# Optimization experiments

Hardware: AMD Instinct MI355X
Metric: run time of the kernel (lower is better)

The kernel has to match this reference:

```python
import jax, jax.numpy as jnp
import numpy as np

N_NODES = 50000


def _gcn_conv(x, src, dst, W, b, n_nodes):
    # x: [N, Fin] -> h: [N, Fout]; GCN: D^-1/2 (A+I) D^-1/2 (x W) + b
    h = x @ W
    deg = jax.ops.segment_sum(jnp.ones_like(dst, dtype=h.dtype), dst,
                              num_segments=n_nodes)
    dinv = jax.lax.rsqrt(jnp.maximum(deg, 1.0))
    norm = dinv[src] * dinv[dst]                      # [E]
    msg = h[src] * norm[:, None]                      # [E, Fout] gather
    agg = jax.ops.segment_sum(msg, dst, num_segments=n_nodes)  # scatter-add
    return agg + b


def setup_inputs() -> dict:
    key = jax.random.key(0)
    k0, k1, k2, k3 = jax.random.split(key, 4)
    N, E, F_IN, H, C = N_NODES, 800000, 128, 128, 16
    x = jax.random.normal(k0, (N, F_IN), dtype=jnp.float32)
    edge_index = jax.random.randint(k1, (2, E), 0, N, dtype=jnp.int64)
    W1 = jax.random.normal(k2, (F_IN, H), dtype=jnp.float32) / np.sqrt(F_IN)
    b1 = jnp.zeros((H,), dtype=jnp.float32)
    W2 = jax.random.normal(k3, (H, C), dtype=jnp.float32) / np.sqrt(H)
    b2 = jnp.zeros((C,), dtype=jnp.float32)
    return {"x": x, "edge_index": edge_index, "W1": W1, "b1": b1,
            "W2": W2, "b2": b2}


def reference(x, edge_index, W1, b1, W2, b2):
    n = x.shape[0]
    # add self-loops (shared by both conv layers)
    loops = jnp.arange(n, dtype=edge_index.dtype)
    src = jnp.concatenate([edge_index[0], loops])
    dst = jnp.concatenate([edge_index[1], loops])
    h = _gcn_conv(x, src, dst, W1, b1, n)
    h = jax.nn.relu(h)
    # dropout p=0.5 is identity in eval mode
    h = _gcn_conv(h, src, dst, W2, b2, n)
    return jax.nn.log_softmax(h, axis=1)
```

## Files before the change

### kernel.cpp

```cpp
#include <hip/hip_runtime.h>
#include <hip/hip_fp16.h>
#include <math.h>


#define NBUCKET_SHIFT 8
#define BIN_CHUNK 4096
#define PAD_SLOP (7 << NBUCKET_SHIFT)
#define CAP  5120
#define CCAP (CAP + PAD_SLOP)

typedef __bf16 bf16x8 __attribute__((ext_vector_type(8)));
typedef float  f32x4  __attribute__((ext_vector_type(4)));
typedef float  f32x2  __attribute__((ext_vector_type(2)));

__device__ __forceinline__ unsigned short pack_bf16(float f) {
    unsigned u = __float_as_uint(f);
    return (unsigned short)((u + 0x7fffu + ((u >> 16) & 1u)) >> 16);
}

__device__ __forceinline__ void acc_fp8x16_fma(f32x2* a, uint4 v, float w) {
    f32x2 ww; ww.x = w; ww.y = w;
    a[0] += __builtin_amdgcn_cvt_pk_f32_fp8(v.x, false) * ww;
    a[1] += __builtin_amdgcn_cvt_pk_f32_fp8(v.x, true)  * ww;
    a[2] += __builtin_amdgcn_cvt_pk_f32_fp8(v.y, false) * ww;
    a[3] += __builtin_amdgcn_cvt_pk_f32_fp8(v.y, true)  * ww;
    a[4] += __builtin_amdgcn_cvt_pk_f32_fp8(v.z, false) * ww;
    a[5] += __builtin_amdgcn_cvt_pk_f32_fp8(v.z, true)  * ww;
    a[6] += __builtin_amdgcn_cvt_pk_f32_fp8(v.w, false) * ww;
    a[7] += __builtin_amdgcn_cvt_pk_f32_fp8(v.w, true)  * ww;
}

__device__ __forceinline__ void acc_fp16x8(f32x2* a, uint4 v) {
    float2 f;
    f = __half22float2(*(const __half2*)&v.x); a[0] += *(f32x2*)&f;
    f = __half22float2(*(const __half2*)&v.y); a[1] += *(f32x2*)&f;
    f = __half22float2(*(const __half2*)&v.z); a[2] += *(f32x2*)&f;
    f = __half22float2(*(const __half2*)&v.w); a[3] += *(f32x2*)&f;
}

union K1Smem {
    struct { unsigned spair[BIN_CHUNK]; int lcnt[256]; int lbase[256]; } b;
    unsigned short wtp[16384];
    float outb[4][16 * 132];
};

__global__ __launch_bounds__(256)
void bin_gemm1_kernel(const int* __restrict__ src, const int* __restrict__ dst,
                      int* __restrict__ bcur, unsigned* __restrict__ pairs,
                      int E, int nbuckets, int nbins,
                      const float* __restrict__ x, const float* __restrict__ W1,
                      unsigned* __restrict__ h1b, int N) {
    __shared__ K1Smem sm;
    const int blk = blockIdx.x;
    const int tid = threadIdx.x;

    if (blk < nbins) {
        const int e0 = blk * BIN_CHUNK;
        const int cnt = min(BIN_CHUNK, E - e0);
        sm.b.lcnt[tid] = 0;
        __syncthreads();
        for (int i = tid; i < cnt; i += 256) {
            unsigned s = (unsigned)src[e0 + i], d = (unsigned)dst[e0 + i];
            sm.b.spair[i] = (d >> NBUCKET_SHIFT) << 24 | (d & 255u) << 16 | s;
            atomicAdd(&sm.b.lcnt[d >> NBUCKET_SHIFT], 1);
        }
        __syncthreads();
        if (tid < nbuckets) {
            int c = sm.b.lcnt[tid];
            sm.b.lbase[tid] = (c > 0) ? atomicAdd(&bcur[tid], c) : 0;
            sm.b.lcnt[tid] = 0;
        }
        __syncthreads();
        for (int i = tid; i < cnt; i += 256) {
            unsigned p = sm.b.spair[i];
            int b = (int)(p >> 24);
            int off = atomicAdd(&sm.b.lcnt[b], 1);
            pairs[b * CAP + sm.b.lbase[b] + off] = p;
        }
        return;
    }

    const int gblk = blk - nbins;
    const int wave = tid >> 6, lane = tid & 63;
    const int q = lane >> 4, m = lane & 15;
    const int row0 = gblk * 64 + wave * 16;
    const int row = row0 + m;
    const int rowc = (row < N) ? row : (N - 1);

    for (int it = tid; it < 16384; it += 256) {
        int k = it >> 7, n = it & 127;
        int t = n >> 4, mm = n & 15;
        int ks = k >> 5;
        int lane2 = (((k & 31) >> 3) << 4) | mm;
        int j = k & 7;
        sm.wtp[(t * 4 + ks) * 512 + lane2 * 8 + j] = pack_bf16(W1[it]);
    }
    __syncthreads();

    f32x4 acc[8];
#pragma unroll
    for (int t = 0; t < 8; t++) acc[t] = (f32x4)0.0f;

#pragma unroll
    for (int ks = 0; ks < 4; ks++) {
        const float4* xp = (const float4*)(x + (size_t)rowc * 128 + ks * 32 + q * 8);
        float4 f0 = xp[0], f1 = xp[1];
        float fv[8] = {f0.x, f0.y, f0.z, f0.w, f1.x, f1.y, f1.z, f1.w};
        bf16x8 ah;
#pragma unroll
        for (int j = 0; j < 8; j++) ah[j] = (__bf16)fv[j];
#pragma unroll
        for (int t = 0; t < 8; t++) {
            bf16x8 b = *(const bf16x8*)(sm.wtp + (size_t)(t * 4 + ks) * 512 + lane * 8);
            acc[t] = __builtin_amdgcn_mfma_f32_16x16x32_bf16(ah, b, acc[t], 0, 0, 0);
        }
    }
    __syncthreads();

#pragma unroll
    for (int t = 0; t < 8; t++)
#pragma unroll
        for (int r = 0; r < 4; r++)
            sm.outb[wave][(q * 4 + r) * 132 + t * 16 + m] = acc[t][r];
    __syncthreads();

    const int r2 = lane >> 2, j = lane & 3;
    const int orow = row0 + r2;
    if (orow < N) {
        const float* lrow = &sm.outb[wave][r2 * 132];
#pragma unroll
        for (int s = 0; s < 4; s++) {
            float4 a = *(const float4*)(lrow + s * 32 + j * 8);
            float4 b = *(const float4*)(lrow + s * 32 + j * 8 + 4);
            unsigned lo = __builtin_amdgcn_cvt_pk_fp8_f32(a.x, a.y, 0, false);
            lo = __builtin_amdgcn_cvt_pk_fp8_f32(a.z, a.w, lo, true);
            unsigned hi = __builtin_amdgcn_cvt_pk_fp8_f32(b.x, b.y, 0, false);
            hi = __builtin_amdgcn_cvt_pk_fp8_f32(b.z, b.w, hi, true);
            ((uint2*)h1b)[((size_t)(s >> 1) * (N + 1) + orow) * 8 + (s & 1) * 4 + j]
                = make_uint2(lo, hi);
        }
    }
}

__global__ __launch_bounds__(256)
void bucket_build_kernel(const int* __restrict__ bcur, const unsigned* __restrict__ pairs,
                         int* __restrict__ rowptr, int* __restrict__ rowcnt,
                         float* __restrict__ dinv, int* __restrict__ colsrc,
                         unsigned* __restrict__ h1b, int N, int nbuckets) {
    __shared__ int cnt[256];
    __shared__ int sm[256];
    const int tid = threadIdx.x;
    const int blk = blockIdx.x;
    const int nb0 = blk << NBUCKET_SHIFT;

    if (blk == 0) {
        if (tid < 16) h1b[((size_t)0 * (N + 1) + N) * 16 + tid] = 0u;
        else if (tid < 32) h1b[((size_t)1 * (N + 1) + N) * 16 + (tid - 16)] = 0u;
        else if (tid == 32) dinv[N] = 0.0f;
    }

    const int lo = blk * CAP;
    const int hi = lo + bcur[blk];
    cnt[tid] = 0;
    __syncthreads();

    for (int i = lo + tid; i < hi; i += 256)
        atomicAdd(&cnt[(int)(pairs[i] >> 16) & 255], 1);
    __syncthreads();

    int v = cnt[tid];
    int pdeg = (v + 7) & ~7;
    sm[tid] = pdeg;
    __syncthreads();
#pragma unroll
    for (int off = 1; off < 256; off <<= 1) {
        int u = (tid >= off) ? sm[tid - off] : 0;
        __syncthreads();
        sm[tid] += u;
        __syncthreads();
    }
    int pexcl = sm[tid] - pdeg;
    const int start = blk * CCAP + pexcl;
    int node = nb0 + tid;
    if (node < N) {
        rowptr[node] = start;
        rowcnt[node] = pdeg;
        dinv[node] = rsqrtf((float)v + 1.0f);
    }
    __syncthreads();
    cnt[tid] = start;
    __syncthreads();
    for (int i = lo + tid; i < hi; i += 256) {
        unsigned p = pairs[i];
        int pos = atomicAdd(&cnt[(int)(p >> 16) & 255], 1);
        colsrc[pos] = (int)(p & 0xffffu);
    }
    for (int p = start + v; p < start + pdeg; ++p)
        colsrc[p] = N;
}

__global__ __launch_bounds__(256)
void l1_fused_kernel(const int* __restrict__ rowptr, const int* __restrict__ rowcnt,
                     const int* __restrict__ colsrc,
                     const float* __restrict__ dinv, const unsigned* __restrict__ h1b,
                     const float* __restrict__ b1, const float* __restrict__ W2,
                     float* __restrict__ h2acc, int N) {
    __shared__ float rows[4][4][68];
    __shared__ float w2s[64 * 16];
    const int tid = threadIdx.x;
    const int wave = tid >> 6, lane = tid & 63;
    const int c = lane & 3;
    const int g = (lane >> 2) & 3;
    const int n = lane >> 4;
    const int p = blockIdx.x & 1;
    const int d = (blockIdx.x >> 1) * 16 + wave * 4 + n;

    for (int i = tid; i < 256; i += 256)
        ((float4*)w2s)[i] = ((const float4*)W2)[p * 256 + i];

    const uint4* hq = (const uint4*)h1b + (size_t)p * (N + 1) * 4;

    if (d < N) {
        const float dvd = dinv[d];
        f32x2 a[8];
#pragma unroll
        for (int j = 0; j < 8; j++) a[j] = (f32x2)0.0f;

        if (g == 0)
            acc_fp8x16_fma(a, hq[(size_t)d * 4 + c], dvd);

        int i = rowptr[d];
        const int end = i + rowcnt[d];
        int s0 = 0, s1 = 0, s2 = 0, s3 = 0;
        if (i + 16 <= end) {
            s0 = colsrc[i + g];      s1 = colsrc[i + g + 4];
            s2 = colsrc[i + g + 8];  s3 = colsrc[i + g + 12];
        }
        while (i + 16 <= end) {
            uint4 v0 = hq[(size_t)s0 * 4 + c];
            uint4 v1 = hq[(size_t)s1 * 4 + c];
            uint4 v2 = hq[(size_t)s2 * 4 + c];
            uint4 v3 = hq[(size_t)s3 * 4 + c];
            float w0 = dinv[s0], w1 = dinv[s1], w2 = dinv[s2], w3 = dinv[s3];
            i += 16;
            if (i + 16 <= end) {
                s0 = colsrc[i + g];      s1 = colsrc[i + g + 4];
                s2 = colsrc[i + g + 8];  s3 = colsrc[i + g + 12];
            }
            acc_fp8x16_fma(a, v0, w0); acc_fp8x16_fma(a, v1, w1);
            acc_fp8x16_fma(a, v2, w2); acc_fp8x16_fma(a, v3, w3);
        }
        for (; i + 4 <= end; i += 4) {
            int sx = colsrc[i + g];
            acc_fp8x16_fma(a, hq[(size_t)sx * 4 + c], dinv[sx]);
        }

#pragma unroll
        for (int j = 0; j < 8; j++) {
            a[j].x += __shfl_xor(a[j].x, 4, 64);
            a[j].y += __shfl_xor(a[j].y, 4, 64);
            a[j].x += __shfl_xor(a[j].x, 8, 64);
            a[j].y += __shfl_xor(a[j].y, 8, 64);
        }

        if (g == 0) {
            float* rbase = &rows[wave][n][c * 16];
#pragma unroll
            for (int t = 0; t < 4; t++) {
                float4 bb = ((const float4*)b1)[p * 16 + c * 4 + t];
                float4 o;
                o.x = fmaxf(a[2 * t].x * dvd + bb.x, 0.0f);
                o.y = fmaxf(a[2 * t].y * dvd + bb.y, 0.0f);
                o.z = fmaxf(a[2 * t + 1].x * dvd + bb.z, 0.0f);
                o.w = fmaxf(a[2 * t + 1].y * dvd + bb.w, 0.0f);
                *(float4*)(rbase + 4 * t) = o;
            }
        }
    }
    __syncthreads();

    const int n2 = lane >> 4, col = lane & 15;
    const int d2 = (blockIdx.x >> 1) * 16 + wave * 4 + n2;
    if (d2 < N) {
        const float* r = &rows[wave][n2][0];
        float p0 = 0.0f, p1 = 0.0f;
#pragma unroll
        for (int k = 0; k < 32; k++) {
            p0 = fmaf(r[k],      w2s[k * 16 + col],        p0);
            p1 = fmaf(r[k + 32], w2s[(k + 32) * 16 + col], p1);
        }
        atomicAdd(&h2acc[(size_t)d2 * 16 + col], p0 + p1);
    }
}

__global__ __launch_bounds__(256)
void h2cvt_kernel(const float* __restrict__ h2acc, const float* __restrict__ dinv,
                  unsigned* __restrict__ h2h, int N) {
    int idx = blockIdx.x * 256 + threadIdx.x;
    if (idx >= (N + 1) * 4) return;
    float dv = dinv[idx >> 2];
    float4 v = ((const float4*)h2acc)[idx];
    __half2 lo = __floats2half2_rn(v.x * dv, v.y * dv);
    __half2 hi = __floats2half2_rn(v.z * dv, v.w * dv);
    ((uint2*)h2h)[idx] = make_uint2(*(unsigned*)&lo, *(unsigned*)&hi);
}

__global__ __launch_bounds__(256)
void l2_kernel(const int* __restrict__ rowptr, const int* __restrict__ rowcnt,
               const int* __restrict__ colsrc,
               const float* __restrict__ dinv, const unsigned* __restrict__ h2s,
               const float* __restrict__ b2, float* __restrict__ out, int N) {
    const int tid = threadIdx.x;
    const int wave = tid >> 6, lane = tid & 63;
    const int n = lane >> 4;
    const int g = (lane >> 1) & 7;
    const int c = lane & 1;
    const int d = blockIdx.x * 16 + wave * 4 + n;
    if (d >= N) return;
    const uint4* h2q = (const uint4*)h2s;

    f32x2 a[4];
#pragma unroll
    for (int j = 0; j < 4; j++) a[j] = (f32x2)0.0f;

    if (g == 0)
        acc_fp16x8(a, h2q[(size_t)d * 2 + c]);

    int i = rowptr[d];
    const int end = i + rowcnt[d];
    uint4 v; int s2 = 0;
    if (i < end) {
        int s = colsrc[i + g];
        v = h2q[(size_t)s * 2 + c];
    }
    if (i + 8 < end) s2 = colsrc[i + 8 + g];
    while (i < end) {
        uint4 vc = v;
        if (i + 8 < end) v = h2q[(size_t)s2 * 2 + c];
        if (i + 16 < end) s2 = colsrc[i + 16 + g];
        i += 8;
        acc_fp16x8(a, vc);
    }

#pragma unroll
    for (int j = 0; j < 4; j++) {
#pragma unroll
        for (int off = 2; off <= 8; off <<= 1) {
            a[j].x += __shfl_xor(a[j].x, off, 64);
            a[j].y += __shfl_xor(a[j].y, off, 64);
        }
    }

    const float dv = dinv[d];
    const float* af = (const float*)a;
    float v8[8];
#pragma unroll
    for (int j = 0; j < 8; j++) v8[j] = af[j] * dv + b2[c * 8 + j];

    float m = v8[0];
#pragma unroll
    for (int j = 1; j < 8; j++) m = fmaxf(m, v8[j]);
    m = fmaxf(m, __shfl_xor(m, 1, 64));
    float e = 0.0f;
#pragma unroll
    for (int j = 0; j < 8; j++) e += expf(v8[j] - m);
    e += __shfl_xor(e, 1, 64);
    float lse = m + logf(e);

    if (g == 0) {
        float4 o0 = make_float4(v8[0] - lse, v8[1] - lse, v8[2] - lse, v8[3] - lse);
        float4 o1 = make_float4(v8[4] - lse, v8[5] - lse, v8[6] - lse, v8[7] - lse);
        float4* op = (float4*)(out + (size_t)d * 16 + c * 8);
        op[0] = o0; op[1] = o1;
    }
}

extern "C" void kernel_launch(void* const* d_in, const int* in_sizes, int n_in,
                              void* d_out, int out_size, void* d_ws, size_t ws_size,
                              hipStream_t stream) {
    const float* x  = (const float*)d_in[0];
    const int*  ei  = (const int*)d_in[1];
    const float* W1 = (const float*)d_in[2];
    const float* b1 = (const float*)d_in[3];
    const float* W2 = (const float*)d_in[4];
    const float* b2 = (const float*)d_in[5];
    float* out = (float*)d_out;

    const int N = in_sizes[0] / 128;
    const int E = in_sizes[1] / 2;
    const int* src = ei;
    const int* dst = ei + E;
    const int nbuckets = (N + 255) >> NBUCKET_SHIFT;
    const int nbins = (E + BIN_CHUNK - 1) / BIN_CHUNK;
    const int g1blocks = (N + 63) / 64;

    float*          wsf     = (float*)d_ws;
    float*          dinv    = wsf;
    int*            rowptr  = (int*)(wsf + N + 16);
    int*            rowcnt  = rowptr + N;
    int*            bcur    = rowcnt + N;
    float*          h2acc   = (float*)(bcur + 256);
    int*            colsrc  = (int*)(h2acc + (size_t)(N + 1) * 16);
    unsigned*       pairs   = (unsigned*)(colsrc + (size_t)nbuckets * CCAP);
    unsigned*       h1b     = pairs + (size_t)nbuckets * CAP;
    unsigned*       h2h     = pairs;

    hipMemsetAsync(bcur, 0, (256 + (size_t)(N + 1) * 16) * sizeof(int), stream);
    bin_gemm1_kernel<<<nbins + g1blocks, 256, 0, stream>>>(src, dst, bcur, pairs,
                                                           E, nbuckets, nbins,
                                                           x, W1, h1b, N);

    bucket_build_kernel<<<nbuckets, 256, 0, stream>>>(bcur, pairs, rowptr, rowcnt,
                                                      dinv, colsrc, h1b, N, nbuckets);

    l1_fused_kernel<<<((N + 15) / 16) * 2, 256, 0, stream>>>(rowptr, rowcnt, colsrc,
                                                             dinv, h1b, b1, W2,
                                                             h2acc, N);

    h2cvt_kernel<<<((N + 1) * 4 + 255) / 256, 256, 0, stream>>>(h2acc, dinv, h2h, N);

    l2_kernel<<<(N + 15) / 16, 256, 0, stream>>>(rowptr, rowcnt, colsrc, dinv, h2h,
                                                 b2, out, N);
}
```

Before: 158.4 us.

## Pack fp16 source norm weight into CSR column entries and precompute degrees

Degrees are now counted with global atomics during edge binning, so the bucket builder no longer makes its own counting pass over the pairs. Each CSR column entry now packs the 16-bit source index with an fp16 copy of that source's inverse-sqrt degree. The layer-1 gather then reads the weight from the column word instead of making a separate random dinv lookup. This trades 800K extra global atomics and an fp16 rounding of the edge weights for one fewer dependent gather per edge.

```diff
diff --git a/kernel.cpp b/kernel.cpp
--- a/kernel.cpp
+++ b/kernel.cpp
@@ -16,6 +16,10 @@
 __device__ __forceinline__ unsigned short pack_bf16(float f) {
     unsigned u = __float_as_uint(f);
     return (unsigned short)((u + 0x7fffu + ((u >> 16) & 1u)) >> 16);
+}
+
+__device__ __forceinline__ float unpack_w(unsigned u) {
+    return __half2float(__ushort_as_half((unsigned short)(u >> 16)));
 }
 
 __device__ __forceinline__ void acc_fp8x16_fma(f32x2* a, uint4 v, float w) {
@@ -47,7 +51,7 @@
 __global__ __launch_bounds__(256)
 void bin_gemm1_kernel(const int* __restrict__ src, const int* __restrict__ dst,
                       int* __restrict__ bcur, unsigned* __restrict__ pairs,
-                      int E, int nbuckets, int nbins,
+                      int* __restrict__ deg, int E, int nbuckets, int nbins,
                       const float* __restrict__ x, const float* __restrict__ W1,
                       unsigned* __restrict__ h1b, int N) {
     __shared__ K1Smem sm;
@@ -63,6 +67,7 @@
             unsigned s = (unsigned)src[e0 + i], d = (unsigned)dst[e0 + i];
             sm.b.spair[i] = (d >> NBUCKET_SHIFT) << 24 | (d & 255u) << 16 | s;
             atomicAdd(&sm.b.lcnt[d >> NBUCKET_SHIFT], 1);
+            atomicAdd(&deg[d], 1);
         }
         __syncthreads();
         if (tid < nbuckets) {
@@ -144,8 +149,9 @@
 
 __global__ __launch_bounds__(256)
 void bucket_build_kernel(const int* __restrict__ bcur, const unsigned* __restrict__ pairs,
+                         const int* __restrict__ deg,
                          int* __restrict__ rowptr, int* __restrict__ rowcnt,
-                         float* __restrict__ dinv, int* __restrict__ colsrc,
+                         float* __restrict__ dinv, unsigned* __restrict__ colsrc,
                          unsigned* __restrict__ h1b, int N, int nbuckets) {
     __shared__ int cnt[256];
     __shared__ int sm[256];
@@ -161,14 +167,9 @@
 
     const int lo = blk * CAP;
     const int hi = lo + bcur[blk];
-    cnt[tid] = 0;
-    __syncthreads();
-
-    for (int i = lo + tid; i < hi; i += 256)
-        atomicAdd(&cnt[(int)(pairs[i] >> 16) & 255], 1);
-    __syncthreads();
-
-    int v = cnt[tid];
+
+    int node = nb0 + tid;
+    int v = (node < N) ? deg[node] : 0;
     int pdeg = (v + 7) & ~7;
     sm[tid] = pdeg;
     __syncthreads();
@@ -181,7 +182,6 @@
     }
     int pexcl = sm[tid] - pdeg;
     const int start = blk * CCAP + pexcl;
-    int node = nb0 + tid;
     if (node < N) {
         rowptr[node] = start;
         rowcnt[node] = pdeg;
@@ -192,16 +192,19 @@
     __syncthreads();
     for (int i = lo + tid; i < hi; i += 256) {
         unsigned p = pairs[i];
+        unsigned s = p & 0xffffu;
         int pos = atomicAdd(&cnt[(int)(p >> 16) & 255], 1);
-        colsrc[pos] = (int)(p & 0xffffu);
+        float w = rsqrtf((float)deg[s] + 1.0f);
+        unsigned w16 = (unsigned)__half_as_ushort(__float2half_rn(w));
+        colsrc[pos] = s | (w16 << 16);
     }
     for (int p = start + v; p < start + pdeg; ++p)
-        colsrc[p] = N;
+        colsrc[p] = (unsigned)N;
 }
 
 __global__ __launch_bounds__(256)
 void l1_fused_kernel(const int* __restrict__ rowptr, const int* __restrict__ rowcnt,
-                     const int* __restrict__ colsrc,
+                     const unsigned* __restrict__ colsrc,
                      const float* __restrict__ dinv, const unsigned* __restrict__ h1b,
                      const float* __restrict__ b1, const float* __restrict__ W2,
                      float* __restrict__ h2acc, int N) {
@@ -231,28 +234,29 @@
 
         int i = rowptr[d];
         const int end = i + rowcnt[d];
-        int s0 = 0, s1 = 0, s2 = 0, s3 = 0;
+        unsigned u0 = 0, u1 = 0, u2 = 0, u3 = 0;
         if (i + 16 <= end) {
-            s0 = colsrc[i + g];      s1 = colsrc[i + g + 4];
-            s2 = colsrc[i + g + 8];  s3 = colsrc[i + g + 12];
+            u0 = colsrc[i + g];      u1 = colsrc[i + g + 4];
+            u2 = colsrc[i + g + 8];  u3 = colsrc[i + g + 12];
         }
         while (i + 16 <= end) {
-            uint4 v0 = hq[(size_t)s0 * 4 + c];
-            uint4 v1 = hq[(size_t)s1 * 4 + c];
-            uint4 v2 = hq[(size_t)s2 * 4 + c];
-            uint4 v3 = hq[(size_t)s3 * 4 + c];
-            float w0 = dinv[s0], w1 = dinv[s1], w2 = dinv[s2], w3 = dinv[s3];
+            uint4 v0 = hq[(size_t)(u0 & 0xffffu) * 4 + c];
+            uint4 v1 = hq[(size_t)(u1 & 0xffffu) * 4 + c];
+            uint4 v2 = hq[(size_t)(u2 & 0xffffu) * 4 + c];
+            uint4 v3 = hq[(size_t)(u3 & 0xffffu) * 4 + c];
+            float w0 = unpack_w(u0), w1 = unpack_w(u1);
+            float w2 = unpack_w(u2), w3 = unpack_w(u3);
             i += 16;
             if (i + 16 <= end) {
-                s0 = colsrc[i + g];      s1 = colsrc[i + g + 4];
-                s2 = colsrc[i + g + 8];  s3 = colsrc[i + g + 12];
+                u0 = colsrc[i + g];      u1 = colsrc[i + g + 4];
+                u2 = colsrc[i + g + 8];  u3 = colsrc[i + g + 12];
             }
             acc_fp8x16_fma(a, v0, w0); acc_fp8x16_fma(a, v1, w1);
             acc_fp8x16_fma(a, v2, w2); acc_fp8x16_fma(a, v3, w3);
         }
         for (; i + 4 <= end; i += 4) {
-            int sx = colsrc[i + g];
-            acc_fp8x16_fma(a, hq[(size_t)sx * 4 + c], dinv[sx]);
+            unsigned ux = colsrc[i + g];
+            acc_fp8x16_fma(a, hq[(size_t)(ux & 0xffffu) * 4 + c], unpack_w(ux));
         }
 
 #pragma unroll
@@ -307,7 +311,7 @@
 
 __global__ __launch_bounds__(256)
 void l2_kernel(const int* __restrict__ rowptr, const int* __restrict__ rowcnt,
-               const int* __restrict__ colsrc,
+               const unsigned* __restrict__ colsrc,
                const float* __restrict__ dinv, const unsigned* __restrict__ h2s,
                const float* __restrict__ b2, float* __restrict__ out, int N) {
     const int tid = threadIdx.x;
@@ -328,16 +332,16 @@
 
     int i = rowptr[d];
     const int end = i + rowcnt[d];
-    uint4 v; int s2 = 0;
+    uint4 v; unsigned u2 = 0;
     if (i < end) {
-        int s = colsrc[i + g];
-        v = h2q[(size_t)s * 2 + c];
-    }
-    if (i + 8 < end) s2 = colsrc[i + 8 + g];
+        unsigned u = colsrc[i + g];
+        v = h2q[(size_t)(u & 0xffffu) * 2 + c];
+    }
+    if (i + 8 < end) u2 = colsrc[i + 8 + g];
     while (i < end) {
         uint4 vc = v;
-        if (i + 8 < end) v = h2q[(size_t)s2 * 2 + c];
-        if (i + 16 < end) s2 = colsrc[i + 16 + g];
+        if (i + 8 < end) v = h2q[(size_t)(u2 & 0xffffu) * 2 + c];
+        if (i + 16 < end) u2 = colsrc[i + 16 + g];
         i += 8;
         acc_fp16x8(a, vc);
     }
@@ -399,19 +403,23 @@
     int*            rowptr  = (int*)(wsf + N + 16);
     int*            rowcnt  = rowptr + N;
     int*            bcur    = rowcnt + N;
-    float*          h2acc   = (float*)(bcur + 256);
-    int*            colsrc  = (int*)(h2acc + (size_t)(N + 1) * 16);
-    unsigned*       pairs   = (unsigned*)(colsrc + (size_t)nbuckets * CCAP);
+    int*            deg     = bcur + 256;
+    float*          h2acc   = (float*)(deg + N + 16);
+    unsigned*       colsrc  = (unsigned*)(h2acc + (size_t)(N + 1) * 16);
+    unsigned*       pairs   = colsrc + (size_t)nbuckets * CCAP;
     unsigned*       h1b     = pairs + (size_t)nbuckets * CAP;
     unsigned*       h2h     = pairs;
 
-    hipMemsetAsync(bcur, 0, (256 + (size_t)(N + 1) * 16) * sizeof(int), stream);
+    const size_t zero_ints = 256 + (size_t)(N + 16) + (size_t)(N + 1) * 16;
+
+    hipMemsetAsync(bcur, 0, zero_ints * sizeof(int), stream);
     bin_gemm1_kernel<<<nbins + g1blocks, 256, 0, stream>>>(src, dst, bcur, pairs,
-                                                           E, nbuckets, nbins,
+                                                           deg, E, nbuckets, nbins,
                                                            x, W1, h1b, N);
 
-    bucket_build_kernel<<<nbuckets, 256, 0, stream>>>(bcur, pairs, rowptr, rowcnt,
-                                                      dinv, colsrc, h1b, N, nbuckets);
+    bucket_build_kernel<<<nbuckets, 256, 0, stream>>>(bcur, pairs, deg, rowptr,
+                                                      rowcnt, dinv, colsrc, h1b,
+                                                      N, nbuckets);
 
     l1_fused_kernel<<<((N + 15) / 16) * 2, 256, 0, stream>>>(rowptr, rowcnt, colsrc,
                                                              dinv, h1b, b1, W2,
```

New measurement: 181.3 us. 14.5% more time.
